# Performance work log

Measured on AMD Instinct MI355X. Metric: run time of the kernel, lower is better.

The kernel has to match this reference:

```python
import jax, jax.numpy as jnp
import numpy as np

K_MASK = jnp.finfo(jnp.bfloat16).min
ROPE_THETA = 1000000.0


def _rope_sincos(position_ids, head_dim, theta):
    # position_ids: [b, t] int -> sin, cos: [b, t, head_dim//2]
    frac = jnp.arange(0, head_dim, 2, dtype=jnp.float32) / head_dim
    timescale = theta ** frac
    ang = position_ids[..., None].astype(jnp.float32) / timescale
    return jnp.sin(ang), jnp.cos(ang)


def _apply_rope(x, sin, cos):
    # x: [b, t, n, h]; sin/cos: [b, t, h//2]
    h = x.shape[-1]
    x1, x2 = x[..., : h // 2], x[..., h // 2 :]
    s = sin[:, :, None, :]
    c = cos[:, :, None, :]
    return jnp.concatenate([x1 * c - x2 * s, x2 * c + x1 * s], axis=-1).astype(x.dtype)


def setup_inputs() -> dict:
    key = jax.random.key(0)
    ks = jax.random.split(key, 8)
    b, t, S = 8, 16, 8192
    D, N, K, H = 1536, 12, 2, 128
    std = 0.01  # nnx.initializers.normal() default stddev
    return {
        "x": jax.random.normal(ks[0], (b, t, D), jnp.float32),
        "k_cache": jax.random.normal(ks[1], (b, S, K, H), jnp.float32),
        "v_cache": jax.random.normal(ks[2], (b, S, K, H), jnp.float32),
        "wq": jax.random.normal(ks[3], (D, N, H), jnp.float32) * std,
        "bq": jnp.zeros((N, H), jnp.float32),
        "wk": jax.random.normal(ks[4], (D, K, H), jnp.float32) * std,
        "bk": jnp.zeros((K, H), jnp.float32),
        "wv": jax.random.normal(ks[5], (D, K, H), jnp.float32) * std,
        "bv": jnp.zeros((K, H), jnp.float32),
        "wo": jax.random.normal(ks[6], (N, H, D), jnp.float32) * std,
        "segment_ids": jnp.ones((b, t), jnp.int32),
        "start_ind": jnp.zeros((8,), jnp.int32),
        "cur_ind": 4096,
    }


def reference(x, k_cache, v_cache, wq, bq, wk, bk, wv, bv, wo,
              segment_ids, start_ind, cur_ind):
    b, t, D = x.shape
    S = k_cache.shape[1]
    N, H = wq.shape[1], wq.shape[2]
    K = wk.shape[1]
    G = N // K  # n_rep
    scale = H ** -0.5

    # projections with bias
    q = jnp.einsum("btd,dnh->btnh", x, wq) + bq
    kp = jnp.einsum("btd,dkh->btkh", x, wk) + bk
    v = jnp.einsum("btd,dkh->btkh", x, wv) + bv

    # left-pad bookkeeping (count_left_pads) and start index resolution
    nonpad = segment_ids != 0  # [b, t]
    left_pads = jnp.argmax(nonpad, axis=-1).astype(jnp.int32)
    start = jnp.where(start_ind < 0, left_pads, start_ind)  # [b]

    # positions from segment ids, offset by current cache index
    positions = jnp.maximum(jnp.cumsum(nonpad.astype(jnp.int32), axis=-1) - 1, 0) + cur_ind
    sin, cos = _rope_sincos(positions, H, ROPE_THETA)
    q = _apply_rope(q, sin, cos)
    kp = _apply_rope(kp, sin, cos)

    # cache update
    k_cache = jax.lax.dynamic_update_slice(k_cache, kp.astype(k_cache.dtype), (0, cur_ind, 0, 0))
    v_cache = jax.lax.dynamic_update_slice(v_cache, v.astype(v_cache.dtype), (0, cur_ind, 0, 0))

    # GQA attention over full cache
    qg = q.reshape(b, t, K, G, H)
    logits = jnp.einsum("btkgh,bskh->btskg", qg, k_cache) * scale  # [b,t,S,K,G]

    q_pos = cur_ind + jnp.arange(t, dtype=jnp.int32)[None, :] - start[:, None]  # [b,t]
    ts = jnp.arange(S, dtype=jnp.int32)
    kv_seg = (ts[None, :] >= start[:, None]) & (ts[None, :] < cur_ind + t)  # [b,S]
    k_pos = ts[None, :] - start[:, None]
    causal = k_pos[:, None, :] <= q_pos[:, :, None]  # [b,t,S]
    seg = kv_seg[:, None, :].astype(segment_ids.dtype) == segment_ids[:, :, None]  # [b,t,S]
    mask = (causal & seg)[:, :, :, None, None]

    logits = jnp.where(mask, logits, K_MASK)
    w = jax.nn.softmax(logits.astype(jnp.float32), axis=2).astype(logits.dtype)
    qkv = jnp.einsum("btskg,bskh->btkgh", w, v_cache).reshape(b, t, N, H)
    return jnp.einsum("btnh,nhd->btd", qkv, wo)
```

## Files before the change

kernel.cpp:

```cpp
#include <hip/hip_runtime.h>

#define B_ 8
#define T_ 16
#define D_ 1536
#define N_ 12
#define KH_ 2
#define G_ 6
#define H_ 128
#define S_ 8192
#define NCHUNK 16
#define SPLITS 8

typedef __attribute__((ext_vector_type(8))) short bf16x8;
typedef __attribute__((ext_vector_type(4))) float f32x4;
typedef __attribute__((ext_vector_type(4))) unsigned short u16x4;

__device__ __forceinline__ unsigned short f2bf(float x) {
    unsigned u = __float_as_uint(x);
    u += 0x7fffu + ((u >> 16) & 1u);
    return (unsigned short)(u >> 16);
}
__device__ __forceinline__ float bf2f(unsigned short h) {
    return __uint_as_float(((unsigned)h) << 16);
}

__global__ __launch_bounds__(256, 4) void gemm_splitk(
    const float* __restrict__ A,
    const float* __restrict__ W0, int n0, int ldb0,
    const float* __restrict__ W1, int n1, int ldb1,
    const float* __restrict__ W2, int ldb2,
    float* __restrict__ part, int NTOT, int Kdim)
{
    __shared__ __align__(16) unsigned short Ah[64][40], Al[64][40];
    __shared__ __align__(16) unsigned short Bh[64][40], Bl[64][40];
    const int tid = threadIdx.x;
    const int wave = tid >> 6, lane = tid & 63;
    const int col = lane & 15, g = lane >> 4;
    const int row0 = blockIdx.y * 64;
    const int c0 = blockIdx.x * 64;
    const int ks = Kdim / gridDim.z;
    const int k0 = blockIdx.z * ks;

    const float* Bp; int ldb, bc0;
    if (c0 < n0)           { Bp = W0; ldb = ldb0; bc0 = c0; }
    else if (c0 < n0 + n1) { Bp = W1; ldb = ldb1; bc0 = c0 - n0; }
    else                   { Bp = W2; ldb = ldb2; bc0 = c0 - n0 - n1; }

    f32x4 acc[4];
#pragma unroll
    for (int nt = 0; nt < 4; ++nt) acc[nt] = (f32x4){0.f, 0.f, 0.f, 0.f};

    for (int kk = 0; kk < ks; kk += 32) {
        __syncthreads();
        if (tid < 128) {
#pragma unroll
            for (int c = tid; c < 512; c += 128) {
                int r = c >> 3, k4 = c & 7;
                float4 v = *(const float4*)&A[(size_t)(row0 + r) * Kdim + k0 + kk + k4 * 4];
                float f[4] = {v.x, v.y, v.z, v.w};
                u16x4 hv, lv;
#pragma unroll
                for (int i = 0; i < 4; ++i) {
                    unsigned short hh = f2bf(f[i]);
                    hv[i] = hh; lv[i] = f2bf(f[i] - bf2f(hh));
                }
                *(u16x4*)&Ah[r][k4 * 4] = hv;
                *(u16x4*)&Al[r][k4 * 4] = lv;
            }
        } else {
            int t2 = tid - 128;
            int kq = t2 >> 4, cq = t2 & 15;
            float a[4][4];
#pragma unroll
            for (int r = 0; r < 4; ++r) {
                float4 v = *(const float4*)&Bp[(size_t)(k0 + kk + kq * 4 + r) * ldb + bc0 + cq * 4];
                a[r][0] = v.x; a[r][1] = v.y; a[r][2] = v.z; a[r][3] = v.w;
            }
#pragma unroll
            for (int cc = 0; cc < 4; ++cc) {
                u16x4 hv, lv;
#pragma unroll
                for (int r = 0; r < 4; ++r) {
                    unsigned short hh = f2bf(a[r][cc]);
                    hv[r] = hh; lv[r] = f2bf(a[r][cc] - bf2f(hh));
                }
                *(u16x4*)&Bh[cq * 4 + cc][kq * 4] = hv;
                *(u16x4*)&Bl[cq * 4 + cc][kq * 4] = lv;
            }
        }
        __syncthreads();

        bf16x8 ah = *(const bf16x8*)&Ah[wave * 16 + col][g * 8];
        bf16x8 al = *(const bf16x8*)&Al[wave * 16 + col][g * 8];
#pragma unroll
        for (int nt = 0; nt < 4; ++nt) {
            bf16x8 bh = *(const bf16x8*)&Bh[nt * 16 + col][g * 8];
            bf16x8 bl = *(const bf16x8*)&Bl[nt * 16 + col][g * 8];
            acc[nt] = __builtin_amdgcn_mfma_f32_16x16x32_bf16(ah, bh, acc[nt], 0, 0, 0);
            acc[nt] = __builtin_amdgcn_mfma_f32_16x16x32_bf16(ah, bl, acc[nt], 0, 0, 0);
            acc[nt] = __builtin_amdgcn_mfma_f32_16x16x32_bf16(al, bh, acc[nt], 0, 0, 0);
        }
    }
#pragma unroll
    for (int nt = 0; nt < 4; ++nt)
#pragma unroll
        for (int j = 0; j < 4; ++j) {
            size_t prow = (size_t)blockIdx.z * 128 + row0 + wave * 16 + g * 4 + j;
            part[prow * NTOT + c0 + nt * 16 + col] = acc[nt][j];
        }
}

__global__ __launch_bounds__(256) void rope_reduce(
    const float* __restrict__ part,
    const float* __restrict__ bq, const float* __restrict__ bk,
    const float* __restrict__ bv,
    const int* __restrict__ seg, const int* __restrict__ curp,
    float* __restrict__ q_rope, float* __restrict__ k_new,
    float* __restrict__ v_new)
{
    const int row = blockIdx.x;
    const int b = row >> 4, t = row & 15;
    const int tid = threadIdx.x;
    __shared__ float S[2048];
    __shared__ float sc[64][2];

    const int CUR = curp[0];
    int c = 0;
    for (int tt = 0; tt <= t; ++tt) c += (seg[b * T_ + tt] != 0) ? 1 : 0;
    int pos = max(c - 1, 0) + CUR;

    if (tid < 64) {
        float frac = (2.0f * tid) / (float)H_;
        float ts = expf(frac * logf(1000000.0f));
        float ang = (float)pos / ts;
        sc[tid][0] = sinf(ang);
        sc[tid][1] = cosf(ang);
    }
    for (int e = tid; e < 2048; e += 256) {
        float s = 0.f;
#pragma unroll
        for (int sp = 0; sp < SPLITS; ++sp)
            s += part[((size_t)sp * 128 + row) * 2048 + e];
        S[e] = s;
    }
    __syncthreads();

    for (int e = tid; e < 768; e += 256) {
        int n = e >> 6, i = e & 63;
        float x1 = S[n * 128 + i] + bq[n * 128 + i];
        float x2 = S[n * 128 + i + 64] + bq[n * 128 + i + 64];
        float s = sc[i][0], co = sc[i][1];
        q_rope[(size_t)row * 1536 + n * 128 + i]      = x1 * co - x2 * s;
        q_rope[(size_t)row * 1536 + n * 128 + i + 64] = x2 * co + x1 * s;
    }
    if (tid < 128) {
        int n = tid >> 6, i = tid & 63;
        float x1 = S[1536 + n * 128 + i] + bk[n * 128 + i];
        float x2 = S[1536 + n * 128 + i + 64] + bk[n * 128 + i + 64];
        float s = sc[i][0], co = sc[i][1];
        k_new[(size_t)row * 256 + n * 128 + i]      = x1 * co - x2 * s;
        k_new[(size_t)row * 256 + n * 128 + i + 64] = x2 * co + x1 * s;
    }
    v_new[(size_t)row * 256 + tid] = S[1792 + tid] + bv[tid];
}

__global__ __launch_bounds__(384, 2) void attn_mfma(
    const float* __restrict__ q_rope, const float* __restrict__ k_new,
    const float* __restrict__ v_new,
    const float* __restrict__ k_cache, const float* __restrict__ v_cache,
    const int* __restrict__ seg, const int* __restrict__ start_ind,
    const int* __restrict__ curp,
    float* __restrict__ part)
{
    const int chunk = blockIdx.x, b = blockIdx.y, kh = blockIdx.z;
    const int tid = threadIdx.x;
    const int wave = tid >> 6, lane = tid & 63;
    const int col = lane & 15, g = lane >> 4;
    const float scale = 0.088388347648318447f;
    const float NEG_INF = -__builtin_inff();

    const int CUR = curp[0];
    const int SPAN = CUR + T_;
    const int CH = (SPAN + NCHUNK - 1) / NCHUNK;
    const int s0 = chunk * CH;
    const int s1 = min(s0 + CH, SPAN);

    int st = start_ind[b];
    if (st < 0) {
        st = 0;
        for (int tt = 0; tt < T_; ++tt)
            if (seg[b * T_ + tt] != 0) { st = tt; break; }
    }

    __shared__ __align__(16) unsigned short K_hi[32][136], K_lo[32][136];
    __shared__ __align__(16) unsigned short Vt_hi[128][40], Vt_lo[128][40];
    __shared__ __align__(16) unsigned short P_hi[6][16][40], P_lo[6][16][40];

    const int qbase = wave * 16;
    const int qi_a = qbase + col;
    const int t_a = (qi_a * 171) >> 10;
    const int gh_a = qi_a - t_a * G_;
    const float* qp = &q_rope[(((size_t)b * T_ + t_a) * N_ + kh * G_ + gh_a) * H_];
    bf16x8 qh[4], ql[4];
#pragma unroll
    for (int ks = 0; ks < 4; ++ks) {
        float4 va = *(const float4*)&qp[ks * 32 + g * 8];
        float4 vb = *(const float4*)&qp[ks * 32 + g * 8 + 4];
        float f[8] = {va.x, va.y, va.z, va.w, vb.x, vb.y, vb.z, vb.w};
#pragma unroll
        for (int i = 0; i < 8; ++i) {
            float xs = f[i] * scale;
            unsigned short hh = f2bf(xs);
            qh[ks][i] = (short)hh;
            ql[ks][i] = (short)f2bf(xs - bf2f(hh));
        }
    }

    int qpos_r[4], segid_r[4];
#pragma unroll
    for (int j = 0; j < 4; ++j) {
        int qi_c = qbase + g * 4 + j;
        int t_c = (qi_c * 171) >> 10;
        segid_r[j] = seg[b * T_ + t_c];
        qpos_r[j] = CUR + t_c - st;
    }

    float m[4], lsum[4];
#pragma unroll
    for (int j = 0; j < 4; ++j) { m[j] = NEG_INF; lsum[j] = 0.f; }
    f32x4 oacc[8];
#pragma unroll
    for (int nt = 0; nt < 8; ++nt) oacc[nt] = (f32x4){0.f, 0.f, 0.f, 0.f};

    for (int stile = s0; stile < s1; stile += 32) {
        __syncthreads();
        for (int c = tid; c < 1024; c += 384) {
            int key = c >> 5, d4 = c & 31;
            int s = stile + key;
            float4 v = {0.f, 0.f, 0.f, 0.f};
            if (s < s1) {
                const float* src = (s < CUR)
                    ? &k_cache[((((size_t)b * S_ + s) * KH_) + kh) * H_ + d4 * 4]
                    : &k_new[((((size_t)b * T_ + (s - CUR)) * KH_) + kh) * H_ + d4 * 4];
                v = *(const float4*)src;
            }
            float f[4] = {v.x, v.y, v.z, v.w};
            u16x4 hv, lv;
#pragma unroll
            for (int i = 0; i < 4; ++i) {
                unsigned short hh = f2bf(f[i]);
                hv[i] = hh; lv[i] = f2bf(f[i] - bf2f(hh));
            }
            *(u16x4*)&K_hi[key][d4 * 4] = hv;
            *(u16x4*)&K_lo[key][d4 * 4] = lv;
        }
        if (tid < 256) {
            int ky4 = tid >> 5, d4 = tid & 31;
            float a[4][4];
#pragma unroll
            for (int r = 0; r < 4; ++r) {
                int s = stile + ky4 * 4 + r;
                float4 v = {0.f, 0.f, 0.f, 0.f};
                if (s < s1) {
                    const float* src = (s < CUR)
                        ? &v_cache[((((size_t)b * S_ + s) * KH_) + kh) * H_ + d4 * 4]
                        : &v_new[((((size_t)b * T_ + (s - CUR)) * KH_) + kh) * H_ + d4 * 4];
                    v = *(const float4*)src;
                }
                a[r][0] = v.x; a[r][1] = v.y; a[r][2] = v.z; a[r][3] = v.w;
            }
#pragma unroll
            for (int dd = 0; dd < 4; ++dd) {
                u16x4 hv, lv;
#pragma unroll
                for (int r = 0; r < 4; ++r) {
                    unsigned short hh = f2bf(a[r][dd]);
                    hv[r] = hh; lv[r] = f2bf(a[r][dd] - bf2f(hh));
                }
                *(u16x4*)&Vt_hi[d4 * 4 + dd][ky4 * 4] = hv;
                *(u16x4*)&Vt_lo[d4 * 4 + dd][ky4 * 4] = lv;
            }
        }
        __syncthreads();

        f32x4 sacc0 = {0.f, 0.f, 0.f, 0.f}, sacc1 = {0.f, 0.f, 0.f, 0.f};
#pragma unroll
        for (int ks = 0; ks < 4; ++ks) {
            bf16x8 k0h = *(const bf16x8*)&K_hi[col][ks * 32 + g * 8];
            bf16x8 k0l = *(const bf16x8*)&K_lo[col][ks * 32 + g * 8];
            bf16x8 k1h = *(const bf16x8*)&K_hi[16 + col][ks * 32 + g * 8];
            bf16x8 k1l = *(const bf16x8*)&K_lo[16 + col][ks * 32 + g * 8];
            sacc0 = __builtin_amdgcn_mfma_f32_16x16x32_bf16(qh[ks], k0h, sacc0, 0, 0, 0);
            sacc0 = __builtin_amdgcn_mfma_f32_16x16x32_bf16(qh[ks], k0l, sacc0, 0, 0, 0);
            sacc0 = __builtin_amdgcn_mfma_f32_16x16x32_bf16(ql[ks], k0h, sacc0, 0, 0, 0);
            sacc1 = __builtin_amdgcn_mfma_f32_16x16x32_bf16(qh[ks], k1h, sacc1, 0, 0, 0);
            sacc1 = __builtin_amdgcn_mfma_f32_16x16x32_bf16(qh[ks], k1l, sacc1, 0, 0, 0);
            sacc1 = __builtin_amdgcn_mfma_f32_16x16x32_bf16(ql[ks], k1h, sacc1, 0, 0, 0);
        }

        float rj[4];
        const int skey0 = stile + col, skey1 = stile + 16 + col;
#pragma unroll
        for (int j = 0; j < 4; ++j) {
            bool v0 = (skey0 < s1) && (skey0 - st <= qpos_r[j]) &&
                      (((skey0 >= st) ? 1 : 0) == segid_r[j]);
            bool v1 = (skey1 < s1) && (skey1 - st <= qpos_r[j]) &&
                      (((skey1 >= st) ? 1 : 0) == segid_r[j]);
            float lg0 = v0 ? sacc0[j] : NEG_INF;
            float lg1 = v1 ? sacc1[j] : NEG_INF;
            float tm = fmaxf(lg0, lg1);
            tm = fmaxf(tm, __shfl_xor(tm, 1));
            tm = fmaxf(tm, __shfl_xor(tm, 2));
            tm = fmaxf(tm, __shfl_xor(tm, 4));
            tm = fmaxf(tm, __shfl_xor(tm, 8));
            float mn = fmaxf(m[j], tm);
            float r, p0, p1;
            if (mn == NEG_INF) { r = 1.f; p0 = 0.f; p1 = 0.f; }
            else {
                r  = __expf(m[j] - mn);
                p0 = __expf(lg0 - mn);
                p1 = __expf(lg1 - mn);
            }
            float ps = p0 + p1;
            ps += __shfl_xor(ps, 1);
            ps += __shfl_xor(ps, 2);
            ps += __shfl_xor(ps, 4);
            ps += __shfl_xor(ps, 8);
            lsum[j] = lsum[j] * r + ps;
            m[j] = mn;
            rj[j] = r;
            int row = g * 4 + j;
            unsigned short h0 = f2bf(p0);
            P_hi[wave][row][col] = h0;
            P_lo[wave][row][col] = f2bf(p0 - bf2f(h0));
            unsigned short h1 = f2bf(p1);
            P_hi[wave][row][16 + col] = h1;
            P_lo[wave][row][16 + col] = f2bf(p1 - bf2f(h1));
        }

#pragma unroll
        for (int nt = 0; nt < 8; ++nt) {
#pragma unroll
            for (int j = 0; j < 4; ++j) oacc[nt][j] *= rj[j];
        }

        bf16x8 pah = *(const bf16x8*)&P_hi[wave][col][g * 8];
        bf16x8 pal = *(const bf16x8*)&P_lo[wave][col][g * 8];
#pragma unroll
        for (int nt = 0; nt < 8; ++nt) {
            bf16x8 vbh = *(const bf16x8*)&Vt_hi[nt * 16 + col][g * 8];
            bf16x8 vbl = *(const bf16x8*)&Vt_lo[nt * 16 + col][g * 8];
            oacc[nt] = __builtin_amdgcn_mfma_f32_16x16x32_bf16(pah, vbh, oacc[nt], 0, 0, 0);
            oacc[nt] = __builtin_amdgcn_mfma_f32_16x16x32_bf16(pah, vbl, oacc[nt], 0, 0, 0);
            oacc[nt] = __builtin_amdgcn_mfma_f32_16x16x32_bf16(pal, vbh, oacc[nt], 0, 0, 0);
        }
    }

    const size_t base_q = (((size_t)chunk * B_ + b) * KH_ + kh) * 96;
#pragma unroll
    for (int j = 0; j < 4; ++j) {
        int qi = qbase + g * 4 + j;
        size_t pb = (base_q + qi) * 132;
        if (col == 0) { part[pb] = m[j]; part[pb + 1] = lsum[j]; }
#pragma unroll
        for (int nt = 0; nt < 8; ++nt)
            part[pb + 2 + nt * 16 + col] = oacc[nt][j];
    }
}

__global__ __launch_bounds__(256) void combine_kernel(
    const float* __restrict__ part, float* __restrict__ qkv)
{
    const int row = blockIdx.x;
    const int b = row >> 4, t = row & 15;
    const int tid = threadIdx.x;
    const int half = tid >> 7, h = tid & 127;
    const size_t cstride = (size_t)B_ * KH_ * 96 * 132;

    for (int nb = 0; nb < N_; nb += 2) {
        int n = nb + half;
        int kh = n / G_, g = n - kh * G_;
        int qi = t * G_ + g;
        size_t base0 = (((size_t)b * KH_ + kh) * 96 + qi) * 132;
        float M = -__builtin_inff();
        for (int c = 0; c < NCHUNK; ++c)
            M = fmaxf(M, part[base0 + c * cstride]);
        float den = 0.f, num = 0.f;
        for (int c = 0; c < NCHUNK; ++c) {
            float mc = part[base0 + c * cstride];
            float e = (M == -__builtin_inff() || mc == -__builtin_inff())
                          ? 0.f : expf(mc - M);
            den += e * part[base0 + c * cstride + 1];
            num += e * part[base0 + c * cstride + 2 + h];
        }
        qkv[(size_t)row * (N_ * H_) + n * H_ + h] = (den > 0.f) ? num / den : 0.f;
    }
}

__global__ __launch_bounds__(256) void sum_reduce(
    const float* __restrict__ part, float* __restrict__ out, int n)
{
    int i = blockIdx.x * 256 + threadIdx.x;
    if (i < n) {
        float s = 0.f;
#pragma unroll
        for (int sp = 0; sp < SPLITS; ++sp) s += part[(size_t)sp * n + i];
        out[i] = s;
    }
}

extern "C" void kernel_launch(void* const* d_in, const int* in_sizes, int n_in,
                              void* d_out, int out_size, void* d_ws, size_t ws_size,
                              hipStream_t stream)
{
    (void)in_sizes; (void)n_in; (void)out_size; (void)ws_size;
    const float* x       = (const float*)d_in[0];
    const float* k_cache = (const float*)d_in[1];
    const float* v_cache = (const float*)d_in[2];
    const float* wq      = (const float*)d_in[3];
    const float* bq      = (const float*)d_in[4];
    const float* wk      = (const float*)d_in[5];
    const float* bk      = (const float*)d_in[6];
    const float* wv      = (const float*)d_in[7];
    const float* bv      = (const float*)d_in[8];
    const float* wo      = (const float*)d_in[9];
    const int*   seg     = (const int*)d_in[10];
    const int*   start_i = (const int*)d_in[11];
    const int*   curp    = (const int*)d_in[12];
    float* out = (float*)d_out;
    float* ws  = (float*)d_ws;

    const size_t PQKV = (size_t)SPLITS * 128 * 2048;
    const size_t QSZ  = (size_t)B_ * T_ * N_ * H_;
    const size_t KSZ  = (size_t)B_ * T_ * KH_ * H_;
    float* partP  = ws;
    float* q_rope = partP + PQKV;
    float* k_new  = q_rope + QSZ;
    float* v_new  = k_new + KSZ;
    float* partA  = v_new + KSZ;
    const size_t PSZ = (size_t)NCHUNK * B_ * KH_ * 96 * 132;
    float* qkv    = partA + PSZ;

    gemm_splitk<<<dim3(32, 2, SPLITS), 256, 0, stream>>>(
        x, wq, 1536, 1536, wk, 256, 256, wv, 256, partP, 2048, D_);

    rope_reduce<<<B_ * T_, 256, 0, stream>>>(partP, bq, bk, bv, seg, curp,
                                             q_rope, k_new, v_new);

    attn_mfma<<<dim3(NCHUNK, B_, KH_), 384, 0, stream>>>(
        q_rope, k_new, v_new, k_cache, v_cache, seg, start_i, curp, partA);

    combine_kernel<<<B_ * T_, 256, 0, stream>>>(partA, qkv);

    gemm_splitk<<<dim3(24, 2, SPLITS), 256, 0, stream>>>(
        qkv, wo, 1536, 1536, wo, 0, 1536, wo, 1536, partP, 1536, N_ * H_);

    sum_reduce<<<(B_ * T_ * D_ + 255) / 256, 256, 0, stream>>>(
        partP, out, B_ * T_ * D_);
}
```

Measured before the change: 107.6 us.

## Prefetch K/V tiles into registers two tiles ahead of compute

Restructures the attention loop so global loads of K and V for later tiles go into register buffers (double-buffered A/B) while the current tile is computed from shared memory. This hides global memory latency behind the MFMA work. It also skips the second 16-key MFMA block when a tile holds 16 or fewer valid keys. The cost is more live registers, which may reduce occupancy.

```diff
diff --git a/kernel.cpp b/kernel.cpp
--- a/kernel.cpp
+++ b/kernel.cpp
@@ -232,42 +232,65 @@
 #pragma unroll
     for (int nt = 0; nt < 8; ++nt) oacc[nt] = (f32x4){0.f, 0.f, 0.f, 0.f};
 
-    for (int stile = s0; stile < s1; stile += 32) {
-        __syncthreads();
-        for (int c = tid; c < 1024; c += 384) {
-            int key = c >> 5, d4 = c & 31;
-            int s = stile + key;
+    const int vky4 = tid >> 5, vd4 = tid & 31;
+
+    auto issueK = [&](float4* kreg, int stile) {
+#pragma unroll
+        for (int i = 0; i < 3; ++i) {
+            int c = tid + i * 384;
             float4 v = {0.f, 0.f, 0.f, 0.f};
-            if (s < s1) {
-                const float* src = (s < CUR)
-                    ? &k_cache[((((size_t)b * S_ + s) * KH_) + kh) * H_ + d4 * 4]
-                    : &k_new[((((size_t)b * T_ + (s - CUR)) * KH_) + kh) * H_ + d4 * 4];
-                v = *(const float4*)src;
-            }
-            float f[4] = {v.x, v.y, v.z, v.w};
-            u16x4 hv, lv;
-#pragma unroll
-            for (int i = 0; i < 4; ++i) {
-                unsigned short hh = f2bf(f[i]);
-                hv[i] = hh; lv[i] = f2bf(f[i] - bf2f(hh));
-            }
-            *(u16x4*)&K_hi[key][d4 * 4] = hv;
-            *(u16x4*)&K_lo[key][d4 * 4] = lv;
-        }
+            if (c < 1024) {
+                int key = c >> 5, d4 = c & 31;
+                int s = stile + key;
+                if (s < s1) {
+                    const float* src = (s < CUR)
+                        ? &k_cache[((((size_t)b * S_ + s) * KH_) + kh) * H_ + d4 * 4]
+                        : &k_new[((((size_t)b * T_ + (s - CUR)) * KH_) + kh) * H_ + d4 * 4];
+                    v = *(const float4*)src;
+                }
+            }
+            kreg[i] = v;
+        }
+    };
+    auto issueV = [&](float4* vreg, int stile) {
         if (tid < 256) {
-            int ky4 = tid >> 5, d4 = tid & 31;
-            float a[4][4];
 #pragma unroll
             for (int r = 0; r < 4; ++r) {
-                int s = stile + ky4 * 4 + r;
+                int s = stile + vky4 * 4 + r;
                 float4 v = {0.f, 0.f, 0.f, 0.f};
                 if (s < s1) {
                     const float* src = (s < CUR)
-                        ? &v_cache[((((size_t)b * S_ + s) * KH_) + kh) * H_ + d4 * 4]
-                        : &v_new[((((size_t)b * T_ + (s - CUR)) * KH_) + kh) * H_ + d4 * 4];
+                        ? &v_cache[((((size_t)b * S_ + s) * KH_) + kh) * H_ + vd4 * 4]
+                        : &v_new[((((size_t)b * T_ + (s - CUR)) * KH_) + kh) * H_ + vd4 * 4];
                     v = *(const float4*)src;
                 }
-                a[r][0] = v.x; a[r][1] = v.y; a[r][2] = v.z; a[r][3] = v.w;
+                vreg[r] = v;
+            }
+        }
+    };
+    auto convertKV = [&](const float4* kreg, const float4* vreg) {
+#pragma unroll
+        for (int i = 0; i < 3; ++i) {
+            int c = tid + i * 384;
+            if (c < 1024) {
+                int key = c >> 5, d4 = c & 31;
+                float f[4] = {kreg[i].x, kreg[i].y, kreg[i].z, kreg[i].w};
+                u16x4 hv, lv;
+#pragma unroll
+                for (int q = 0; q < 4; ++q) {
+                    unsigned short hh = f2bf(f[q]);
+                    hv[q] = hh; lv[q] = f2bf(f[q] - bf2f(hh));
+                }
+                *(u16x4*)&K_hi[key][d4 * 4] = hv;
+                *(u16x4*)&K_lo[key][d4 * 4] = lv;
+            }
+        }
+        if (tid < 256) {
+            float a[4][4];
+#pragma unroll
+            for (int r = 0; r < 4; ++r) {
+                a[r][0] = vreg[r].x; a[r][1] = vreg[r].y;
+                a[r][2] = vreg[r].z; a[r][3] = vreg[r].w;
             }
 #pragma unroll
             for (int dd = 0; dd < 4; ++dd) {
@@ -277,25 +300,32 @@
                     unsigned short hh = f2bf(a[r][dd]);
                     hv[r] = hh; lv[r] = f2bf(a[r][dd] - bf2f(hh));
                 }
-                *(u16x4*)&Vt_hi[d4 * 4 + dd][ky4 * 4] = hv;
-                *(u16x4*)&Vt_lo[d4 * 4 + dd][ky4 * 4] = lv;
-            }
-        }
-        __syncthreads();
-
+                *(u16x4*)&Vt_hi[vd4 * 4 + dd][vky4 * 4] = hv;
+                *(u16x4*)&Vt_lo[vd4 * 4 + dd][vky4 * 4] = lv;
+            }
+        }
+    };
+
+    auto computeTile = [&](int stile) {
+        const bool full = (s1 - stile) > 16;
         f32x4 sacc0 = {0.f, 0.f, 0.f, 0.f}, sacc1 = {0.f, 0.f, 0.f, 0.f};
 #pragma unroll
         for (int ks = 0; ks < 4; ++ks) {
             bf16x8 k0h = *(const bf16x8*)&K_hi[col][ks * 32 + g * 8];
             bf16x8 k0l = *(const bf16x8*)&K_lo[col][ks * 32 + g * 8];
-            bf16x8 k1h = *(const bf16x8*)&K_hi[16 + col][ks * 32 + g * 8];
-            bf16x8 k1l = *(const bf16x8*)&K_lo[16 + col][ks * 32 + g * 8];
             sacc0 = __builtin_amdgcn_mfma_f32_16x16x32_bf16(qh[ks], k0h, sacc0, 0, 0, 0);
             sacc0 = __builtin_amdgcn_mfma_f32_16x16x32_bf16(qh[ks], k0l, sacc0, 0, 0, 0);
             sacc0 = __builtin_amdgcn_mfma_f32_16x16x32_bf16(ql[ks], k0h, sacc0, 0, 0, 0);
-            sacc1 = __builtin_amdgcn_mfma_f32_16x16x32_bf16(qh[ks], k1h, sacc1, 0, 0, 0);
-            sacc1 = __builtin_amdgcn_mfma_f32_16x16x32_bf16(qh[ks], k1l, sacc1, 0, 0, 0);
-            sacc1 = __builtin_amdgcn_mfma_f32_16x16x32_bf16(ql[ks], k1h, sacc1, 0, 0, 0);
+        }
+        if (full) {
+#pragma unroll
+            for (int ks = 0; ks < 4; ++ks) {
+                bf16x8 k1h = *(const bf16x8*)&K_hi[16 + col][ks * 32 + g * 8];
+                bf16x8 k1l = *(const bf16x8*)&K_lo[16 + col][ks * 32 + g * 8];
+                sacc1 = __builtin_amdgcn_mfma_f32_16x16x32_bf16(qh[ks], k1h, sacc1, 0, 0, 0);
+                sacc1 = __builtin_amdgcn_mfma_f32_16x16x32_bf16(qh[ks], k1l, sacc1, 0, 0, 0);
+                sacc1 = __builtin_amdgcn_mfma_f32_16x16x32_bf16(ql[ks], k1h, sacc1, 0, 0, 0);
+            }
         }
 
         float rj[4];
@@ -353,6 +383,35 @@
             oacc[nt] = __builtin_amdgcn_mfma_f32_16x16x32_bf16(pah, vbh, oacc[nt], 0, 0, 0);
             oacc[nt] = __builtin_amdgcn_mfma_f32_16x16x32_bf16(pah, vbl, oacc[nt], 0, 0, 0);
             oacc[nt] = __builtin_amdgcn_mfma_f32_16x16x32_bf16(pal, vbh, oacc[nt], 0, 0, 0);
+        }
+    };
+
+    const int ntiles = (s1 - s0 + 31) >> 5;
+    float4 kregA[3], vregA[4], kregB[3], vregB[4];
+
+    issueK(kregA, s0); issueV(vregA, s0);
+    if (ntiles > 1) { issueK(kregB, s0 + 32); issueV(vregB, s0 + 32); }
+
+    for (int ti = 0; ti < ntiles; ti += 2) {
+        {
+            convertKV(kregA, vregA);
+            __syncthreads();
+            if (ti + 2 < ntiles) {
+                issueK(kregA, s0 + (ti + 2) * 32);
+                issueV(vregA, s0 + (ti + 2) * 32);
+            }
+            computeTile(s0 + ti * 32);
+            __syncthreads();
+        }
+        if (ti + 1 < ntiles) {
+            convertKV(kregB, vregB);
+            __syncthreads();
+            if (ti + 3 < ntiles) {
+                issueK(kregB, s0 + (ti + 3) * 32);
+                issueV(vregB, s0 + (ti + 3) * 32);
+            }
+            computeTile(s0 + (ti + 1) * 32);
+            __syncthreads();
         }
     }
 
```

New measurement: 95.23 us. 11.5% less time.

## Load K/V straight into registers with prefetch and drop P·V split-bf16 terms

Applied to the files above, without the earlier changes.

The attention kernel no longer stages K through shared memory. Each wave loads its K fragments directly from global memory into registers, converts them to hi/lo bf16 in place, and prefetches the next tile's K while softmax runs. V is loaded per wave and transposed through a private shared buffer, which removes the block-wide __syncthreads. The P·V product now uses single bf16 P and V (1 MFMA instead of 3), cutting compute and LDS traffic at the cost of accuracy. The 2-blocks occupancy hint is removed and workspace buffers are aliased to shrink the footprint. Each wave now loads K/V redundantly, which raises global/L2 traffic.

```diff
diff --git a/kernel.cpp b/kernel.cpp
--- a/kernel.cpp
+++ b/kernel.cpp
@@ -1,4 +1,5 @@
 #include <hip/hip_runtime.h>
+#include <hip/hip_bf16.h>
 
 #define B_ 8
 #define T_ 16
@@ -164,7 +165,7 @@
     v_new[(size_t)row * 256 + tid] = S[1792 + tid] + bv[tid];
 }
 
-__global__ __launch_bounds__(384, 2) void attn_mfma(
+__global__ __launch_bounds__(384) void attn_mfma(
     const float* __restrict__ q_rope, const float* __restrict__ k_new,
     const float* __restrict__ v_new,
     const float* __restrict__ k_cache, const float* __restrict__ v_cache,
@@ -192,9 +193,8 @@
             if (seg[b * T_ + tt] != 0) { st = tt; break; }
     }
 
-    __shared__ __align__(16) unsigned short K_hi[32][136], K_lo[32][136];
-    __shared__ __align__(16) unsigned short Vt_hi[128][40], Vt_lo[128][40];
-    __shared__ __align__(16) unsigned short P_hi[6][16][40], P_lo[6][16][40];
+    __shared__ __align__(16) unsigned short Vt[6][128][32];
+    __shared__ __align__(16) unsigned short Pl[6][16][40];
 
     const int qbase = wave * 16;
     const int qi_a = qbase + col;
@@ -232,71 +232,75 @@
 #pragma unroll
     for (int nt = 0; nt < 8; ++nt) oacc[nt] = (f32x4){0.f, 0.f, 0.f, 0.f};
 
-    for (int stile = s0; stile < s1; stile += 32) {
-        __syncthreads();
-        for (int c = tid; c < 1024; c += 384) {
-            int key = c >> 5, d4 = c & 31;
-            int s = stile + key;
-            float4 v = {0.f, 0.f, 0.f, 0.f};
-            if (s < s1) {
-                const float* src = (s < CUR)
-                    ? &k_cache[((((size_t)b * S_ + s) * KH_) + kh) * H_ + d4 * 4]
-                    : &k_new[((((size_t)b * T_ + (s - CUR)) * KH_) + kh) * H_ + d4 * 4];
-                v = *(const float4*)src;
-            }
-            float f[4] = {v.x, v.y, v.z, v.w};
-            u16x4 hv, lv;
-#pragma unroll
-            for (int i = 0; i < 4; ++i) {
-                unsigned short hh = f2bf(f[i]);
-                hv[i] = hh; lv[i] = f2bf(f[i] - bf2f(hh));
-            }
-            *(u16x4*)&K_hi[key][d4 * 4] = hv;
-            *(u16x4*)&K_lo[key][d4 * 4] = lv;
-        }
-        if (tid < 256) {
-            int ky4 = tid >> 5, d4 = tid & 31;
-            float a[4][4];
-#pragma unroll
-            for (int r = 0; r < 4; ++r) {
-                int s = stile + ky4 * 4 + r;
-                float4 v = {0.f, 0.f, 0.f, 0.f};
-                if (s < s1) {
-                    const float* src = (s < CUR)
-                        ? &v_cache[((((size_t)b * S_ + s) * KH_) + kh) * H_ + d4 * 4]
-                        : &v_new[((((size_t)b * T_ + (s - CUR)) * KH_) + kh) * H_ + d4 * 4];
-                    v = *(const float4*)src;
+    auto krow = [&](int s) -> const float* {
+        s = min(s, SPAN - 1);
+        return (s < CUR)
+            ? &k_cache[((((size_t)b * S_ + s) * KH_) + kh) * H_]
+            : &k_new[((((size_t)b * T_ + (s - CUR)) * KH_) + kh) * H_];
+    };
+    auto vrow = [&](int s) -> const float* {
+        s = min(s, SPAN - 1);
+        return (s < CUR)
+            ? &v_cache[((((size_t)b * S_ + s) * KH_) + kh) * H_]
+            : &v_new[((((size_t)b * T_ + (s - CUR)) * KH_) + kh) * H_];
+    };
+
+    auto loadK = [&](float4* kf, int stile) {
+#pragma unroll
+        for (int kt = 0; kt < 2; ++kt) {
+            const float* kr = krow(stile + kt * 16 + col);
+#pragma unroll
+            for (int ks = 0; ks < 4; ++ks) {
+                kf[kt * 8 + ks * 2 + 0] = *(const float4*)(kr + ks * 32 + g * 8);
+                kf[kt * 8 + ks * 2 + 1] = *(const float4*)(kr + ks * 32 + g * 8 + 4);
+            }
+        }
+    };
+    auto loadV = [&](float4* vf, int stile) {
+#pragma unroll
+        for (int r = 0; r < 8; ++r) {
+            const float* vr = vrow(stile + g * 8 + r);
+            vf[r * 2 + 0] = *(const float4*)(vr + col * 8);
+            vf[r * 2 + 1] = *(const float4*)(vr + col * 8 + 4);
+        }
+    };
+
+    const int ntiles = (s1 - s0 + 31) >> 5;
+    float4 kf[16], vf[16];
+    loadK(kf, s0);
+
+    for (int ti = 0; ti < ntiles; ++ti) {
+        const int stile = s0 + ti * 32;
+        loadV(vf, stile);
+
+        f32x4 sacc0 = {0.f, 0.f, 0.f, 0.f}, sacc1 = {0.f, 0.f, 0.f, 0.f};
+#pragma unroll
+        for (int kt = 0; kt < 2; ++kt) {
+#pragma unroll
+            for (int ks = 0; ks < 4; ++ks) {
+                float4 a = kf[kt * 8 + ks * 2], bb = kf[kt * 8 + ks * 2 + 1];
+                float f[8] = {a.x, a.y, a.z, a.w, bb.x, bb.y, bb.z, bb.w};
+                union { bf16x8 v; __hip_bfloat162 h2[4]; } Hh, Ll;
+#pragma unroll
+                for (int i = 0; i < 4; ++i) {
+                    float2 p = make_float2(f[2 * i], f[2 * i + 1]);
+                    Hh.h2[i] = __float22bfloat162_rn(p);
+                    float2 q = __bfloat1622float2(Hh.h2[i]);
+                    Ll.h2[i] = __float22bfloat162_rn(make_float2(p.x - q.x, p.y - q.y));
                 }
-                a[r][0] = v.x; a[r][1] = v.y; a[r][2] = v.z; a[r][3] = v.w;
-            }
-#pragma unroll
-            for (int dd = 0; dd < 4; ++dd) {
-                u16x4 hv, lv;
-#pragma unroll
-                for (int r = 0; r < 4; ++r) {
-                    unsigned short hh = f2bf(a[r][dd]);
-                    hv[r] = hh; lv[r] = f2bf(a[r][dd] - bf2f(hh));
+                if (kt == 0) {
+                    sacc0 = __builtin_amdgcn_mfma_f32_16x16x32_bf16(qh[ks], Hh.v, sacc0, 0, 0, 0);
+                    sacc0 = __builtin_amdgcn_mfma_f32_16x16x32_bf16(ql[ks], Hh.v, sacc0, 0, 0, 0);
+                    sacc0 = __builtin_amdgcn_mfma_f32_16x16x32_bf16(qh[ks], Ll.v, sacc0, 0, 0, 0);
+                } else {
+                    sacc1 = __builtin_amdgcn_mfma_f32_16x16x32_bf16(qh[ks], Hh.v, sacc1, 0, 0, 0);
+                    sacc1 = __builtin_amdgcn_mfma_f32_16x16x32_bf16(ql[ks], Hh.v, sacc1, 0, 0, 0);
+                    sacc1 = __builtin_amdgcn_mfma_f32_16x16x32_bf16(qh[ks], Ll.v, sacc1, 0, 0, 0);
                 }
-                *(u16x4*)&Vt_hi[d4 * 4 + dd][ky4 * 4] = hv;
-                *(u16x4*)&Vt_lo[d4 * 4 + dd][ky4 * 4] = lv;
-            }
-        }
-        __syncthreads();
-
-        f32x4 sacc0 = {0.f, 0.f, 0.f, 0.f}, sacc1 = {0.f, 0.f, 0.f, 0.f};
-#pragma unroll
-        for (int ks = 0; ks < 4; ++ks) {
-            bf16x8 k0h = *(const bf16x8*)&K_hi[col][ks * 32 + g * 8];
-            bf16x8 k0l = *(const bf16x8*)&K_lo[col][ks * 32 + g * 8];
-            bf16x8 k1h = *(const bf16x8*)&K_hi[16 + col][ks * 32 + g * 8];
-            bf16x8 k1l = *(const bf16x8*)&K_lo[16 + col][ks * 32 + g * 8];
-            sacc0 = __builtin_amdgcn_mfma_f32_16x16x32_bf16(qh[ks], k0h, sacc0, 0, 0, 0);
-            sacc0 = __builtin_amdgcn_mfma_f32_16x16x32_bf16(qh[ks], k0l, sacc0, 0, 0, 0);
-            sacc0 = __builtin_amdgcn_mfma_f32_16x16x32_bf16(ql[ks], k0h, sacc0, 0, 0, 0);
-            sacc1 = __builtin_amdgcn_mfma_f32_16x16x32_bf16(qh[ks], k1h, sacc1, 0, 0, 0);
-            sacc1 = __builtin_amdgcn_mfma_f32_16x16x32_bf16(qh[ks], k1l, sacc1, 0, 0, 0);
-            sacc1 = __builtin_amdgcn_mfma_f32_16x16x32_bf16(ql[ks], k1h, sacc1, 0, 0, 0);
-        }
+            }
+        }
+
+        if (ti + 1 < ntiles) loadK(kf, stile + 32);
 
         float rj[4];
         const int skey0 = stile + col, skey1 = stile + 16 + col;
@@ -330,12 +334,8 @@
             m[j] = mn;
             rj[j] = r;
             int row = g * 4 + j;
-            unsigned short h0 = f2bf(p0);
-            P_hi[wave][row][col] = h0;
-            P_lo[wave][row][col] = f2bf(p0 - bf2f(h0));
-            unsigned short h1 = f2bf(p1);
-            P_hi[wave][row][16 + col] = h1;
-            P_lo[wave][row][16 + col] = f2bf(p1 - bf2f(h1));
+            Pl[wave][row][col]      = f2bf(p0);
+            Pl[wave][row][16 + col] = f2bf(p1);
         }
 
 #pragma unroll
@@ -344,15 +344,24 @@
             for (int j = 0; j < 4; ++j) oacc[nt][j] *= rj[j];
         }
 
-        bf16x8 pah = *(const bf16x8*)&P_hi[wave][col][g * 8];
-        bf16x8 pal = *(const bf16x8*)&P_lo[wave][col][g * 8];
+#pragma unroll
+        for (int c = 0; c < 8; ++c) {
+            float fr[8];
+#pragma unroll
+            for (int r = 0; r < 8; ++r)
+                fr[r] = ((const float*)&vf[r * 2 + (c >> 2)])[c & 3];
+            union { bf16x8 v; __hip_bfloat162 h2[4]; } W;
+#pragma unroll
+            for (int i = 0; i < 4; ++i)
+                W.h2[i] = __float22bfloat162_rn(make_float2(fr[2 * i], fr[2 * i + 1]));
+            *(bf16x8*)&Vt[wave][(c << 4) | col][g * 8] = W.v;
+        }
+
+        bf16x8 pa = *(const bf16x8*)&Pl[wave][col][g * 8];
 #pragma unroll
         for (int nt = 0; nt < 8; ++nt) {
-            bf16x8 vbh = *(const bf16x8*)&Vt_hi[nt * 16 + col][g * 8];
-            bf16x8 vbl = *(const bf16x8*)&Vt_lo[nt * 16 + col][g * 8];
-            oacc[nt] = __builtin_amdgcn_mfma_f32_16x16x32_bf16(pah, vbh, oacc[nt], 0, 0, 0);
-            oacc[nt] = __builtin_amdgcn_mfma_f32_16x16x32_bf16(pah, vbl, oacc[nt], 0, 0, 0);
-            oacc[nt] = __builtin_amdgcn_mfma_f32_16x16x32_bf16(pal, vbh, oacc[nt], 0, 0, 0);
+            bf16x8 vb = *(const bf16x8*)&Vt[wave][((col & 7) << 4) | (nt * 2) | (col >> 3)][g * 8];
+            oacc[nt] = __builtin_amdgcn_mfma_f32_16x16x32_bf16(pa, vb, oacc[nt], 0, 0, 0);
         }
     }
 
@@ -430,16 +439,15 @@
     float* out = (float*)d_out;
     float* ws  = (float*)d_ws;
 
-    const size_t PQKV = (size_t)SPLITS * 128 * 2048;
+    const size_t PSZ  = (size_t)NCHUNK * B_ * KH_ * 96 * 132;
     const size_t QSZ  = (size_t)B_ * T_ * N_ * H_;
     const size_t KSZ  = (size_t)B_ * T_ * KH_ * H_;
     float* partP  = ws;
-    float* q_rope = partP + PQKV;
+    float* partA  = ws;
+    float* q_rope = ws + PSZ;
     float* k_new  = q_rope + QSZ;
     float* v_new  = k_new + KSZ;
-    float* partA  = v_new + KSZ;
-    const size_t PSZ = (size_t)NCHUNK * B_ * KH_ * 96 * 132;
-    float* qkv    = partA + PSZ;
+    float* qkv    = v_new + KSZ;
 
     gemm_splitk<<<dim3(32, 2, SPLITS), 256, 0, stream>>>(
         x, wq, 1536, 1536, wk, 256, 256, wv, 256, partP, 2048, D_);
```

After: 98.80 us. 1.09x faster.
